# Performance work log

Hardware: AMD Instinct MI355X
Metric: run time of the kernel (lower is better)

## Reference

```python
import jax, jax.numpy as jnp
import numpy as np
from math import sqrt

B, L, DM, H, NL, INTER = 4, 2048, 256, 8, 3, 16
E = DM // H
FACTOR = 5


def _ln(x, g, b, eps=1e-5):
    m = x.mean(-1, keepdims=True)
    v = ((x - m) ** 2).mean(-1, keepdims=True)
    return (x - m) * jax.lax.rsqrt(v + eps) * g + b


def _prob_attn(q, k, v, rkey):
    # q,k,v: [B,H,L,E]; ProbAttention with mask_flag=False (as in AttentionLayer)
    Bq, Hq, Lq, Eq = q.shape
    Lk = k.shape[2]
    U = min(FACTOR * int(np.ceil(np.log(Lk))), Lk)   # sample_k
    u = min(FACTOR * int(np.ceil(np.log(Lq))), Lq)   # n_top
    # random K indices shared across B,H as in torch randint(L_K,(L_Q,sample_k))
    idx = jax.random.randint(rkey, (Lq, U), 0, Lk)
    k_samp = k[:, :, idx, :]                                   # [B,H,Lq,U,E]
    qk_samp = jnp.einsum('bhle,bhlue->bhlu', q, k_samp)        # [B,H,Lq,U]
    M = qk_samp.max(-1) - qk_samp.sum(-1) / Lk                 # sparsity score
    _, top = jax.lax.top_k(M, u)                               # [B,H,u]
    q_red = jnp.take_along_axis(q, top[..., None], axis=2)     # [B,H,u,E]
    scores = jnp.einsum('bhue,bhke->bhuk', q_red, k) * (1.0 / sqrt(Eq))
    attn = jax.nn.softmax(scores, axis=-1)
    upd = jnp.einsum('bhuk,bhkd->bhud', attn, v)               # [B,H,u,E]
    # initial context = mean of V broadcast over queries (non-masked branch)
    ctx = jnp.broadcast_to(v.mean(axis=2, keepdims=True), (Bq, Hq, Lq, Eq))
    bi = jnp.arange(Bq)[:, None, None]
    hi = jnp.arange(Hq)[None, :, None]
    ctx = ctx.at[bi, hi, top].set(upd)
    return ctx.transpose(0, 2, 1, 3)                           # [B,L,H,E]


def _enc_layer(x, wq, bq, wk, bk, wv, bv, wo, bo, c1w, c1b, c2w, c2b, g1, b1, g2, b2, rkey):
    Bx, Lx, _ = x.shape
    qh = (x @ wq.T + bq).reshape(Bx, Lx, H, E).transpose(0, 2, 1, 3)
    kh = (x @ wk.T + bk).reshape(Bx, Lx, H, E).transpose(0, 2, 1, 3)
    vh = (x @ wv.T + bv).reshape(Bx, Lx, H, E).transpose(0, 2, 1, 3)
    ctx = _prob_attn(qh, kh, vh, rkey).reshape(Bx, Lx, DM)
    x = _ln(x + ctx @ wo.T + bo, g1, b1)
    y = jax.nn.relu(jnp.einsum('bld,fd->blf', x, c1w) + c1b)   # 1x1 conv
    y = jnp.einsum('blf,df->bld', y, c2w) + c2b                # 1x1 conv
    return _ln(x + y, g2, b2)


def _distill(x, w, cb, g, b):
    # circular Conv1d(k=3,pad=1) + BatchNorm1d (train stats) + ELU; MaxPool(k=1) = identity
    xt = x.transpose(0, 2, 1)                                  # [B,C,L]
    xp = jnp.concatenate([xt[..., -1:], xt, xt[..., :1]], axis=-1)
    y = jax.lax.conv_general_dilated(xp, w, (1,), 'VALID',
                                     dimension_numbers=('NCH', 'OIH', 'NCH')) + cb[None, :, None]
    m = y.mean(axis=(0, 2), keepdims=True)
    v = y.var(axis=(0, 2), keepdims=True)                      # biased var, torch BN training
    y = jax.nn.elu((y - m) * jax.lax.rsqrt(v + 1e-5) * g[None, :, None] + b[None, :, None])
    return y.transpose(0, 2, 1)


def _forward(x, wq, bq, wk, bk, wv, bv, wo, bo, c1w, c1b, c2w, c2b,
             ln1g, ln1b, ln2g, ln2b, dcw, dcb, bng, bnb, fng, fnb):
    base = jax.random.key(42)
    for i in range(NL - 1):
        x = _enc_layer(x, wq[i], bq[i], wk[i], bk[i], wv[i], bv[i], wo[i], bo[i],
                       c1w[i], c1b[i], c2w[i], c2b[i], ln1g[i], ln1b[i], ln2g[i], ln2b[i],
                       jax.random.fold_in(base, i))
        x = _distill(x, dcw[i], dcb[i], bng[i], bnb[i])
    i = NL - 1
    x = _enc_layer(x, wq[i], bq[i], wk[i], bk[i], wv[i], bv[i], wo[i], bo[i],
                   c1w[i], c1b[i], c2w[i], c2b[i], ln1g[i], ln1b[i], ln2g[i], ln2b[i],
                   jax.random.fold_in(base, i))
    return _ln(x, fng, fnb)


def setup_inputs():
    key = jax.random.key(0)
    ks = jax.random.split(key, 10)
    g = lambda k, shp, s: jax.random.normal(k, shp, jnp.float32) * s
    z = lambda shp: jnp.zeros(shp, jnp.float32)
    o = lambda shp: jnp.ones(shp, jnp.float32)
    return {
        'x': g(ks[0], (B, L, DM), 1.0),
        'wq': g(ks[1], (NL, DM, DM), 0.03), 'bq': z((NL, DM)),
        'wk': g(ks[2], (NL, DM, DM), 0.03), 'bk': z((NL, DM)),
        'wv': g(ks[3], (NL, DM, DM), 0.03), 'bv': z((NL, DM)),
        'wo': g(ks[4], (NL, DM, DM), 0.03), 'bo': z((NL, DM)),
        'c1w': g(ks[5], (NL, INTER, DM), 0.05), 'c1b': z((NL, INTER)),
        'c2w': g(ks[6], (NL, DM, INTER), 0.05), 'c2b': z((NL, DM)),
        'ln1g': o((NL, DM)), 'ln1b': z((NL, DM)),
        'ln2g': o((NL, DM)), 'ln2b': z((NL, DM)),
        'dcw': g(ks[7], (NL - 1, DM, DM, 3), 0.02), 'dcb': z((NL - 1, DM)),
        'bng': o((NL - 1, DM)), 'bnb': z((NL - 1, DM)),
        'fng': o((DM,)), 'fnb': z((DM,)),
    }


def reference(x, wq, bq, wk, bk, wv, bv, wo, bo, c1w, c1b, c2w, c2b,
              ln1g, ln1b, ln2g, ln2b, dcw, dcb, bng, bnb, fng, fnb):
    return _forward(x, wq, bq, wk, bk, wv, bv, wo, bo, c1w, c1b, c2w, c2b,
                    ln1g, ln1b, ln2g, ln2b, dcw, dcb, bng, bnb, fng, fnb)
```

## Files before the change

### kernel.cpp

```cpp
#include <hip/hip_runtime.h>
#include <stdint.h>

#define BB 4
#define LL 2048
#define DMM 256
#define HH 8
#define EE 32
#define NLL 3
#define ITR 16
#define UU 40
#define KC 16
#define KCH 128
#define ROWS (BB*LL)
#define NELEM (ROWS*DMM)
#define OTR 32

typedef __attribute__((ext_vector_type(8))) short short8;
typedef __attribute__((ext_vector_type(4))) float f32x4;
typedef unsigned long long u64;

#define GLDS16(g, l)                                                        \
  __builtin_amdgcn_global_load_lds(                                         \
      (const __attribute__((address_space(1))) uint32_t*)(g),               \
      (__attribute__((address_space(3))) uint32_t*)(l), 16, 0, 0)

__device__ __forceinline__ float bfbits(unsigned short u) {
  return __uint_as_float(((uint32_t)u) << 16);
}
__device__ __forceinline__ unsigned short f2b(float f) {
  uint32_t u = __float_as_uint(f);
  uint32_t r = (u + 0x7FFFu + ((u >> 16) & 1u)) >> 16;
  return (unsigned short)r;
}

__host__ __device__ inline void threefry2x32(uint32_t k0, uint32_t k1,
                                             uint32_t x0, uint32_t x1,
                                             uint32_t* o0, uint32_t* o1) {
  uint32_t ks2 = k0 ^ k1 ^ 0x1BD11BDAu;
  x0 += k0; x1 += k1;
#define TFR(r) { x0 += x1; x1 = (x1 << (r)) | (x1 >> (32 - (r))); x1 ^= x0; }
  TFR(13) TFR(15) TFR(26) TFR(6)
  x0 += k1;  x1 += ks2 + 1u;
  TFR(17) TFR(29) TFR(16) TFR(24)
  x0 += ks2; x1 += k0 + 2u;
  TFR(13) TFR(15) TFR(26) TFR(6)
  x0 += k0;  x1 += k1 + 3u;
  TFR(17) TFR(29) TFR(16) TFR(24)
  x0 += k1;  x1 += ks2 + 4u;
  TFR(13) TFR(15) TFR(26) TFR(6)
  x0 += ks2; x1 += k0 + 5u;
#undef TFR
  *o0 = x0; *o1 = x1;
}

__device__ __forceinline__ float wave_sum(float v) {
#pragma unroll
  for (int off = 32; off > 0; off >>= 1) v += __shfl_xor(v, off);
  return v;
}

struct CvtArgs {
  const void* src[23];
  float* dstF[23];
  unsigned short* dstB[23];
  unsigned short* dstL[23];
  int n[23];
  int blkStart[24];
  unsigned short* dcwT;
  float* vmpZ;
  int* flagOut;
};
__global__ __launch_bounds__(256) void mega_cvt(CvtArgs a) {
  __shared__ int cnt;
  if (threadIdx.x == 0) cnt = 0;
  __syncthreads();
  {
    const unsigned short* u = (const unsigned short*)a.src[0];
    int bad = 0;
#pragma unroll
    for (int rep = 0; rep < 2; ++rep) {
      float v = bfbits(u[threadIdx.x + 256 * rep]);
      float av = fabsf(v);
      bool ok = (v == 0.0f) || (av > 1e-4f && av < 100.0f);
      if (!ok) bad++;
    }
    if (bad) atomicAdd(&cnt, bad);
  }
  __syncthreads();
  int isf32 = (cnt > 25) ? 1 : 0;

  int bid = blockIdx.x;
  if (bid == a.blkStart[23]) {
    for (int t = threadIdx.x; t < BB * DMM; t += 256) a.vmpZ[t] = 0.f;
    if (threadIdx.x == 0) *a.flagOut = isf32;
    return;
  }
  int i = 0;
  while (i < 22 && bid >= a.blkStart[i + 1]) ++i;
  int e = (bid - a.blkStart[i]) * 256 + (int)threadIdx.x;
  if (e >= a.n[i]) return;
  float v; unsigned short rw;
  if (isf32) { v = ((const float*)a.src[i])[e]; rw = f2b(v); }
  else       { rw = ((const unsigned short*)a.src[i])[e]; v = bfbits(rw); }
  a.dstF[i][e] = v;
  if (a.dstB[i]) a.dstB[i][e] = rw;
  if (a.dstL[i]) a.dstL[i][e] = f2b(v - bfbits(rw));
  if (i == 17) {
    int ly = e / 196608;
    int r = e - ly * 196608;
    int n = r / 768;
    int rem = r - n * 768;
    int k = rem / 3, t = rem - k * 3;
    a.dcwT[ly * 196608 + t * 65536 + n * 256 + k] = rw;
  }
}

struct QKVArgs {
  const unsigned short* W[3];
  const float* bias[3];
  float* Cq;
  float* Ck;
  unsigned short* Cv;
  float* vmp;
};
__global__ __launch_bounds__(256) void gemm_qkv(const unsigned short* __restrict__ Ahi,
                                                const unsigned short* __restrict__ Alo,
                                                QKVArgs qa) {
  __shared__ __attribute__((aligned(16))) unsigned short AsH[128][32];
  __shared__ __attribute__((aligned(16))) unsigned short AsL[128][32];
  __shared__ __attribute__((aligned(16))) unsigned short Bs[64][32];
  int z = blockIdx.z;
  const unsigned short* W = qa.W[z];
  const float* bias = qa.bias[z];
  bool twoPass = (z < 2);
  int bm = blockIdx.x * 128, bn = blockIdx.y * 64;
  int tid = threadIdx.x;
  int wv = tid >> 6, lane = tid & 63;
  int wm = wv >> 1, wn = wv & 1;
  int l15 = lane & 15, quad = lane >> 4;
  int lrow = lane >> 2, lseg = lane & 3;
  f32x4 acc[4][2];
#pragma unroll
  for (int i = 0; i < 4; ++i)
#pragma unroll
    for (int j = 0; j < 2; ++j) acc[i][j] = (f32x4){0.f, 0.f, 0.f, 0.f};
  for (int k0 = 0; k0 < 256; k0 += 32) {
    __syncthreads();
#pragma unroll
    for (int s = 0; s < 2; ++s) {
      int brow = (wv + s * 4) * 16;
      size_t goff = (size_t)(bm + brow + lrow) * 256 + k0 + lseg * 8;
      GLDS16(Ahi + goff, &AsH[brow][0]);
      if (twoPass) GLDS16(Alo + goff, &AsL[brow][0]);
    }
    {
      int brow = wv * 16;
      GLDS16(W + (size_t)(bn + brow + lrow) * 256 + k0 + lseg * 8, &Bs[brow][0]);
    }
    __syncthreads();
    short8 ah[4], bfr[2];
#pragma unroll
    for (int mt = 0; mt < 4; ++mt)
      ah[mt] = *(const short8*)(&AsH[wm * 64 + mt * 16 + l15][quad * 8]);
#pragma unroll
    for (int nt = 0; nt < 2; ++nt)
      bfr[nt] = *(const short8*)(&Bs[wn * 32 + nt * 16 + l15][quad * 8]);
#pragma unroll
    for (int mt = 0; mt < 4; ++mt)
#pragma unroll
      for (int nt = 0; nt < 2; ++nt)
        acc[mt][nt] = __builtin_amdgcn_mfma_f32_16x16x32_bf16(ah[mt], bfr[nt],
                                                              acc[mt][nt], 0, 0, 0);
    if (twoPass) {
      short8 al[4];
#pragma unroll
      for (int mt = 0; mt < 4; ++mt)
        al[mt] = *(const short8*)(&AsL[wm * 64 + mt * 16 + l15][quad * 8]);
#pragma unroll
      for (int mt = 0; mt < 4; ++mt)
#pragma unroll
        for (int nt = 0; nt < 2; ++nt)
          acc[mt][nt] = __builtin_amdgcn_mfma_f32_16x16x32_bf16(al[mt], bfr[nt],
                                                                acc[mt][nt], 0, 0, 0);
    }
  }
  float* C = (z == 0) ? qa.Cq : qa.Ck;
#pragma unroll
  for (int nt = 0; nt < 2; ++nt) {
    int n = bn + wn * 32 + nt * 16 + l15;
    float bv = bias[n];
    float csum = 0.f;
#pragma unroll
    for (int mt = 0; mt < 4; ++mt)
#pragma unroll
      for (int r = 0; r < 4; ++r) {
        int m = bm + wm * 64 + mt * 16 + quad * 4 + r;
        float val = acc[mt][nt][r] + bv;
        if (z < 2) {
          C[(size_t)m * 256 + n] = val;
        } else {
          qa.Cv[(size_t)m * 256 + n] = f2b(val);
          csum += val;
        }
      }
    if (z == 2) {
      csum += __shfl_xor(csum, 16);
      csum += __shfl_xor(csum, 32);
      if (quad == 0) {
        int b = bm >> 11;
        atomicAdd(&qa.vmp[b * DMM + n], csum);
      }
    }
  }
}

__global__ __launch_bounds__(512) void oproj_tail(const float* __restrict__ vmp,
                                                  const unsigned char* __restrict__ mapb,
                                                  const float* __restrict__ pm,
                                                  const float* __restrict__ pl,
                                                  const float* __restrict__ po,
                                                  const unsigned short* __restrict__ W,
                                                  const float* __restrict__ bias,
                                                  const float* __restrict__ X,
                                                  const float* __restrict__ g1,
                                                  const float* __restrict__ b1ln,
                                                  const float* __restrict__ w1,
                                                  const float* __restrict__ b1,
                                                  const float* __restrict__ w2,
                                                  const float* __restrict__ b2,
                                                  const float* __restrict__ g2,
                                                  const float* __restrict__ b2ln,
                                                  float* __restrict__ Out,
                                                  unsigned short* __restrict__ OutB,
                                                  unsigned short* __restrict__ OutL,
                                                  const float* __restrict__ fing,
                                                  const float* __restrict__ finb,
                                                  void* __restrict__ finOut,
                                                  const int* __restrict__ flag,
                                                  float* __restrict__ stpZ,
                                                  float* __restrict__ stp2Z) {
  __shared__ __attribute__((aligned(16))) unsigned short As[OTR][DMM];
  __shared__ __attribute__((aligned(16))) unsigned short Bs[256][32];
  __shared__ float Cs[OTR][DMM];
  __shared__ float xs[8][DMM];
  int tid = threadIdx.x;
  if (blockIdx.x == 0 && tid < DMM) {
    stpZ[tid] = 0.f;
    stp2Z[tid] = 0.f;
  }
  int bm = blockIdx.x * OTR;
  int wv = tid >> 6, lane = tid & 63;
  int l15 = lane & 15, quad = lane >> 4;
  int b = bm >> 11, l0 = bm & 2047;
  const float invL = 1.0f / (float)LL;

#pragma unroll
  for (int uu = 0; uu < 2; ++uu) {
    int u = tid * 2 + uu;
    int arow = u >> 5;
    int sub = u & 31;
    int h = sub >> 2, adg = sub & 3;
    int bh = b * HH + h;
    int l = l0 + arow;
    int q = (int)mapb[bh * 2048 + l];
    unsigned short outv[8];
    if (q) {
      size_t base = ((size_t)bh * UU + (q - 1)) * KC;
      float Mx = -1e30f;
#pragma unroll
      for (int kc = 0; kc < KC; ++kc) Mx = fmaxf(Mx, pm[base + kc]);
      float Ls = 0.f;
      float sc[KC];
#pragma unroll
      for (int kc = 0; kc < KC; ++kc) {
        sc[kc] = expf(pm[base + kc] - Mx);
        Ls += pl[base + kc] * sc[kc];
      }
      float inv = 1.0f / Ls;
#pragma unroll
      for (int j = 0; j < 8; ++j) {
        int dl = adg * 8 + j;
        float o = 0.f;
#pragma unroll
        for (int kc = 0; kc < KC; ++kc) o += po[(base + kc) * 32 + dl] * sc[kc];
        outv[j] = f2b(o * inv);
      }
    } else {
      const float* vp = vmp + b * DMM + h * EE + adg * 8;
#pragma unroll
      for (int j = 0; j < 8; ++j) outv[j] = f2b(vp[j] * invL);
    }
    *(uint4*)(&As[arow][h * EE + adg * 8]) = *(const uint4*)outv;
  }
  __syncthreads();

  f32x4 acc[2][2];
#pragma unroll
  for (int i = 0; i < 2; ++i)
#pragma unroll
    for (int j = 0; j < 2; ++j) acc[i][j] = (f32x4){0.f, 0.f, 0.f, 0.f};
  for (int k0 = 0; k0 < 256; k0 += 32) {
    if (k0) __syncthreads();
    {
      int lrw = lane >> 2, lsg = lane & 3;
#pragma unroll
      for (int s = 0; s < 2; ++s) {
        int brow = s * 128 + wv * 16;
        GLDS16(W + (size_t)(brow + lrw) * 256 + k0 + lsg * 8, &Bs[brow][0]);
      }
    }
    __syncthreads();
    short8 af[2], bfr[2];
#pragma unroll
    for (int mt = 0; mt < 2; ++mt)
      af[mt] = *(const short8*)(&As[mt * 16 + l15][k0 + quad * 8]);
#pragma unroll
    for (int nt = 0; nt < 2; ++nt)
      bfr[nt] = *(const short8*)(&Bs[wv * 32 + nt * 16 + l15][quad * 8]);
#pragma unroll
    for (int mt = 0; mt < 2; ++mt)
#pragma unroll
      for (int nt = 0; nt < 2; ++nt)
        acc[mt][nt] = __builtin_amdgcn_mfma_f32_16x16x32_bf16(af[mt], bfr[nt],
                                                              acc[mt][nt], 0, 0, 0);
  }
#pragma unroll
  for (int nt = 0; nt < 2; ++nt) {
    int n = wv * 32 + nt * 16 + l15;
    float bv = bias[n];
#pragma unroll
    for (int mt = 0; mt < 2; ++mt)
#pragma unroll
      for (int r = 0; r < 4; ++r)
        Cs[mt * 16 + quad * 4 + r][n] = acc[mt][nt][r] + bv;
  }
  __syncthreads();
  for (int rr = 0; rr < 4; ++rr) {
    int lr = wv * 4 + rr;
    size_t row = (size_t)bm + lr;
    const float* xr = X + row * DMM;
    const float* tr = Cs[lr];
    float v[4];
#pragma unroll
    for (int i = 0; i < 4; ++i) v[i] = xr[lane + 64 * i] + tr[lane + 64 * i];
    float s = wave_sum(v[0] + v[1] + v[2] + v[3]);
    float m = s * (1.0f / (float)DMM);
    float sq = 0.f;
#pragma unroll
    for (int i = 0; i < 4; ++i) { float d = v[i] - m; sq += d * d; }
    sq = wave_sum(sq);
    float rstd = rsqrtf(sq * (1.0f / (float)DMM) + 1e-5f);
    float xv[4];
#pragma unroll
    for (int i = 0; i < 4; ++i) {
      int d = lane + 64 * i;
      xv[i] = (v[i] - m) * rstd * g1[d] + b1ln[d];
      xs[wv][d] = xv[i];
    }
    __syncthreads();
    int f = lane & 15, qtr = lane >> 4;
    const float* w1p = w1 + f * DMM + qtr * 64;
    const float* xq = &xs[wv][qtr * 64];
    float pacc = 0.f;
#pragma unroll 8
    for (int d = 0; d < 64; ++d) pacc += xq[d] * w1p[d];
    pacc += __shfl_xor(pacc, 16);
    pacc += __shfl_xor(pacc, 32);
    float y1 = fmaxf(pacc + b1[f], 0.0f);
    float y1v[16];
#pragma unroll
    for (int ff = 0; ff < 16; ++ff) y1v[ff] = __shfl(y1, ff);
#pragma unroll
    for (int i = 0; i < 4; ++i) {
      int d = lane + 64 * i;
      const float* w2p = w2 + d * ITR;
      float a = b2[d];
#pragma unroll
      for (int ff = 0; ff < 16; ++ff) a += y1v[ff] * w2p[ff];
      v[i] = xv[i] + a;
    }
    s = wave_sum(v[0] + v[1] + v[2] + v[3]);
    m = s * (1.0f / (float)DMM);
    sq = 0.f;
#pragma unroll
    for (int i = 0; i < 4; ++i) { float d = v[i] - m; sq += d * d; }
    sq = wave_sum(sq);
    rstd = rsqrtf(sq * (1.0f / (float)DMM) + 1e-5f);
    float vv[4];
#pragma unroll
    for (int i = 0; i < 4; ++i) {
      int d = lane + 64 * i;
      float val = (v[i] - m) * rstd * g2[d] + b2ln[d];
      vv[i] = val;
      Out[row * DMM + d] = val;
      unsigned short hi = f2b(val);
      OutB[row * DMM + d] = hi;
      OutL[row * DMM + d] = f2b(val - bfbits(hi));
    }
    if (finOut) {
      s = wave_sum(vv[0] + vv[1] + vv[2] + vv[3]);
      m = s * (1.0f / (float)DMM);
      sq = 0.f;
#pragma unroll
      for (int i = 0; i < 4; ++i) { float d = vv[i] - m; sq += d * d; }
      sq = wave_sum(sq);
      rstd = rsqrtf(sq * (1.0f / (float)DMM) + 1e-5f);
      int isf32 = *flag;
#pragma unroll
      for (int i = 0; i < 4; ++i) {
        int d = lane + 64 * i;
        float val = (vv[i] - m) * rstd * fing[d] + finb[d];
        if (isf32) ((float*)finOut)[row * DMM + d] = val;
        else       ((unsigned short*)finOut)[row * DMM + d] = f2b(val);
      }
    }
  }
}

__global__ __launch_bounds__(256) void gemm_conv(const unsigned short* __restrict__ A,
                                                 const unsigned short* __restrict__ W,
                                                 const float* __restrict__ bias,
                                                 float* __restrict__ C,
                                                 float* __restrict__ stp,
                                                 float* __restrict__ stp2) {
  __shared__ __attribute__((aligned(16))) unsigned short As[80][32];
  __shared__ __attribute__((aligned(16))) unsigned short Bs[192][32];
  int bm = blockIdx.x * 64, bn = blockIdx.y * 64;
  int tid = threadIdx.x;
  int wv = tid >> 6, lane = tid & 63;
  int wm = wv >> 1, wn = wv & 1;
  int l15 = lane & 15, quad = lane >> 4;
  int lrow = lane >> 2, lseg = lane & 3;
  int bbase = bm & ~2047, l0 = bm & 2047;
  f32x4 acc[2][2];
#pragma unroll
  for (int i = 0; i < 2; ++i)
#pragma unroll
    for (int j = 0; j < 2; ++j) acc[i][j] = (f32x4){0.f, 0.f, 0.f, 0.f};
  for (int k0 = 0; k0 < 256; k0 += 32) {
    __syncthreads();
    for (int c = wv; c < 5; c += 4) {
      int i0 = c * 16;
      int l = (l0 - 1 + i0 + lrow + 2048) & 2047;
      GLDS16(A + (size_t)(bbase | l) * 256 + k0 + lseg * 8, &As[i0][0]);
    }
    for (int c = wv; c < 12; c += 4) {
      int i0 = c * 16;
      int tap = c >> 2, brow = (c & 3) * 16;
      GLDS16(W + (size_t)tap * 65536 + (size_t)(bn + brow + lrow) * 256 + k0 + lseg * 8,
             &Bs[i0][0]);
    }
    __syncthreads();
#pragma unroll
    for (int tap = 0; tap < 3; ++tap) {
      short8 af[2], bfr[2];
#pragma unroll
      for (int mt = 0; mt < 2; ++mt)
        af[mt] = *(const short8*)(&As[wm * 32 + mt * 16 + l15 + tap][quad * 8]);
#pragma unroll
      for (int nt = 0; nt < 2; ++nt)
        bfr[nt] = *(const short8*)(&Bs[tap * 64 + wn * 32 + nt * 16 + l15][quad * 8]);
#pragma unroll
      for (int mt = 0; mt < 2; ++mt)
#pragma unroll
        for (int nt = 0; nt < 2; ++nt)
          acc[mt][nt] = __builtin_amdgcn_mfma_f32_16x16x32_bf16(af[mt], bfr[nt],
                                                                acc[mt][nt], 0, 0, 0);
    }
  }
#pragma unroll
  for (int nt = 0; nt < 2; ++nt) {
    int n = bn + wn * 32 + nt * 16 + l15;
    float bv = bias[n];
    float s = 0.f, s2 = 0.f;
#pragma unroll
    for (int mt = 0; mt < 2; ++mt)
#pragma unroll
      for (int r = 0; r < 4; ++r) {
        int m = bm + wm * 32 + mt * 16 + quad * 4 + r;
        float val = acc[mt][nt][r] + bv;
        C[(size_t)m * 256 + n] = val;
        s += val;
        s2 += val * val;
      }
    s  += __shfl_xor(s, 16);   s  += __shfl_xor(s, 32);
    s2 += __shfl_xor(s2, 16);  s2 += __shfl_xor(s2, 32);
    if (quad == 0) {
      atomicAdd(&stp[n], s);
      atomicAdd(&stp2[n], s2);
    }
  }
}

__global__ __launch_bounds__(256) void m_kernel3(const float* __restrict__ Q,
                                                 const float* __restrict__ K,
                                                 uint32_t k20, uint32_t k21,
                                                 float* __restrict__ M) {
  int bid = blockIdx.x;
  int blk = (bid & 7) * 256 + (bid >> 3);
  int b = blk >> 9, lc = blk & 511;
  int wave = threadIdx.x >> 6, lane = threadIdx.x & 63;
  int l = lc * 4 + wave;
  int myidx = 0;
  if (lane < UU) {
    int j = l * UU + lane;
    uint32_t o0, o1;
    const int half = (LL * UU) / 2;
    if (j < half) {
      threefry2x32(k20, k21, (uint32_t)j, (uint32_t)(j + half), &o0, &o1);
      myidx = (int)(o0 & (LL - 1));
    } else {
      threefry2x32(k20, k21, (uint32_t)(j - half), (uint32_t)j, &o0, &o1);
      myidx = (int)(o1 & (LL - 1));
    }
  }
  float4 q4 = *(const float4*)(Q + ((size_t)(b * LL + l)) * DMM + lane * 4);
  const float* Kb = K + (size_t)b * LL * DMM;
  float mx = -1e30f, sm = 0.f;
#pragma unroll 8
  for (int u = 0; u < UU; ++u) {
    int kidx = __shfl(myidx, u);
    float4 k4 = *(const float4*)(Kb + (size_t)kidx * DMM + lane * 4);
    float s = q4.x * k4.x + q4.y * k4.y + q4.z * k4.z + q4.w * k4.w;
    s += __shfl_xor(s, 1);
    s += __shfl_xor(s, 2);
    s += __shfl_xor(s, 4);
    mx = fmaxf(mx, s);
    sm += s;
  }
  if ((lane & 7) == 0) {
    int h = lane >> 3;
    M[((size_t)(b * HH + h)) * LL + l] = mx - sm * (1.0f / (float)LL);
  }
}

__global__ __launch_bounds__(256) void attn_part(const float* __restrict__ Q,
                                                 const float* __restrict__ K,
                                                 const unsigned short* __restrict__ Vbf,
                                                 const float* __restrict__ M,
                                                 unsigned char* __restrict__ mapb,
                                                 float* __restrict__ pm,
                                                 float* __restrict__ pl,
                                                 float* __restrict__ po) {
  __shared__ float Qs[40][32];
  __shared__ unsigned short ps[40][KCH];
  __shared__ unsigned short Vs[KCH][40];
  __shared__ int qrows[40];
  __shared__ unsigned int hist[256];
  __shared__ unsigned int sA[256];
  __shared__ unsigned int sB[256];
  __shared__ unsigned int tbv;
  int kc = blockIdx.x, bh = blockIdx.y;
  int h = bh & 7, b = bh >> 3;
  int tid = threadIdx.x;
  int wv = tid >> 6, lane = tid & 63;

  {
    int row = tid >> 1, half = tid & 1;
    const unsigned short* vsrc =
        Vbf + (size_t)(b * LL + kc * KCH + row) * DMM + h * EE + half * 16;
    *(uint4*)(&Vs[row][half * 16]) = *(const uint4*)vsrc;
    *(uint4*)(&Vs[row][half * 16 + 8]) = *(const uint4*)(vsrc + 8);
  }
  int kk = tid & (KCH - 1), qh = tid >> 7;
  float4 kr[8];
  {
    const float4* kp =
        (const float4*)(K + ((size_t)(b * LL + kc * KCH + kk)) * DMM + h * EE);
#pragma unroll
    for (int j = 0; j < 8; ++j) kr[j] = kp[j];
  }

  u64 kreg[8];
#pragma unroll
  for (int r = 0; r < 8; ++r) {
    int l = tid + 256 * r;
    float v = M[(size_t)bh * LL + l];
    uint32_t bits = __float_as_uint(v);
    uint32_t kv = (bits & 0x80000000u) ? ~bits : (bits | 0x80000000u);
    kreg[r] = ((u64)kv << 32) | (uint32_t)(2047 - l);
  }
  u64 prefix = 0;
  int rank = UU;
  for (int round = 0; round < 8; ++round) {
    int shift = 56 - 8 * round;
    u64 maskTop = (round == 0) ? 0ull : (~0ull << (64 - 8 * round));
    hist[tid] = 0;
    __syncthreads();
#pragma unroll
    for (int r = 0; r < 8; ++r) {
      u64 k = kreg[r];
      if ((k & maskTop) == prefix)
        atomicAdd(&hist[(unsigned int)((k >> shift) & 0xFFu)], 1u);
    }
    __syncthreads();
    sA[tid] = hist[tid];
    __syncthreads();
    unsigned int* src = sA;
    unsigned int* dst = sB;
    for (int off = 1; off < 256; off <<= 1) {
      unsigned int v = src[tid] + ((tid + off < 256) ? src[tid + off] : 0u);
      dst[tid] = v;
      __syncthreads();
      unsigned int* tmpp = src; src = dst; dst = tmpp;
    }
    unsigned int Sb = src[tid];
    unsigned int Snext = (tid < 255) ? src[tid + 1] : 0u;
    if (Sb >= (unsigned int)rank && Snext < (unsigned int)rank) tbv = (unsigned int)tid;
    __syncthreads();
    unsigned int tb = tbv;
    unsigned int above = (tb < 255u) ? src[tb + 1] : 0u;
    rank -= (int)above;
    prefix |= ((u64)tb) << shift;
    __syncthreads();
  }
  u64 T = prefix;
  int myCnt = 0;
#pragma unroll
  for (int r = 0; r < 8; ++r) myCnt += (kreg[r] >= T) ? 1 : 0;
  sA[tid] = (unsigned int)myCnt;
  __syncthreads();
  {
    unsigned int* src = sA;
    unsigned int* dst = sB;
    for (int off = 1; off < 256; off <<= 1) {
      unsigned int v = src[tid] + ((tid >= off) ? src[tid - off] : 0u);
      dst[tid] = v;
      __syncthreads();
      unsigned int* tmpp = src; src = dst; dst = tmpp;
    }
    int pos = (int)src[tid] - myCnt;
    bool wmap = (kc == 0);
#pragma unroll
    for (int r = 0; r < 8; ++r) {
      u64 k = kreg[r];
      int l = 2047 - (int)(uint32_t)(k & 0xFFFFFFFFu);
      unsigned char mv = 0;
      if (k >= T) {
        qrows[pos] = l;
        mv = (unsigned char)(pos + 1);
        pos++;
      }
      if (wmap) mapb[bh * 2048 + l] = mv;
    }
  }
  __syncthreads();

  for (int t = tid; t < 40 * 32; t += 256) {
    int q = t >> 5, d = t & 31;
    Qs[q][d] = Q[((size_t)(b * LL + qrows[q])) * DMM + h * EE + d];
  }
  __syncthreads();
  {
    const float scale = 0.17677669529663687f;
    for (int q = qh * 20; q < qh * 20 + 20; ++q) {
      const float4* qp = (const float4*)Qs[q];
      float s = 0.f;
#pragma unroll
      for (int j = 0; j < 8; ++j) {
        float4 qv = qp[j];
        s += qv.x * kr[j].x + qv.y * kr[j].y + qv.z * kr[j].z + qv.w * kr[j].w;
      }
      ps[q][kk] = f2b(s * scale);
    }
  }
  __syncthreads();
  int kg = lane >> 5, d = lane & 31;
  for (int qq = 0; qq < 10; ++qq) {
    int q = wv * 10 + qq;
    float mx = fmaxf(bfbits(ps[q][lane]), bfbits(ps[q][lane + 64]));
#pragma unroll
    for (int off = 32; off > 0; off >>= 1) mx = fmaxf(mx, __shfl_xor(mx, off));
    float e0 = expf(bfbits(ps[q][lane]) - mx);
    float e1 = expf(bfbits(ps[q][lane + 64]) - mx);
    ps[q][lane] = f2b(e0);
    ps[q][lane + 64] = f2b(e1);
    float sum = wave_sum(e0 + e1);
    float o = 0.f;
#pragma unroll 8
    for (int j = 0; j < KCH / 2; ++j) {
      int r = 2 * j + kg;
      o += bfbits(ps[q][r]) * bfbits(Vs[r][d]);
    }
    o += __shfl_xor(o, 32);
    size_t base = ((size_t)bh * UU + q) * KC + kc;
    if (lane == 0) { pm[base] = mx; pl[base] = sum; }
    if (lane < 32) po[base * 32 + d] = o;
  }
}

__global__ __launch_bounds__(256) void bn_elu(const float* __restrict__ Y,
                                              const float* __restrict__ stp,
                                              const float* __restrict__ stp2,
                                              const float* __restrict__ g,
                                              const float* __restrict__ bb,
                                              float* __restrict__ X,
                                              unsigned short* __restrict__ XB,
                                              unsigned short* __restrict__ XL,
                                              float* __restrict__ vmpZ) {
  int gid = blockIdx.x * 256 + threadIdx.x;
  if (gid < BB * DMM) vmpZ[gid] = 0.f;
  int d = gid & 255;
  float mean = stp[d] * (1.0f / (float)ROWS);
  float var = stp2[d] * (1.0f / (float)ROWS) - mean * mean;
  float rstd = rsqrtf(var + 1e-5f);
  float v = (Y[gid] - mean) * rstd * g[d] + bb[d];
  float r = v > 0.f ? v : expm1f(v);
  X[gid] = r;
  unsigned short hi = f2b(r);
  XB[gid] = hi;
  XL[gid] = f2b(r - bfbits(hi));
}

extern "C" void kernel_launch(void* const* d_in, const int* in_sizes, int n_in,
                              void* d_out, int out_size, void* d_ws, size_t ws_size,
                              hipStream_t stream) {
  (void)in_sizes; (void)n_in; (void)out_size; (void)ws_size;

  float* xbuf = (float*)d_ws;
  float* kb   = xbuf + NELEM;
  float* qb   = kb + NELEM;
  float* tmp  = qb;
  float* Mbuf = qb + NELEM;
  float* vmp  = Mbuf + BB * HH * LL;
  float* stp  = vmp + BB * DMM;
  float* stp2 = stp + DMM;
  float* wp   = stp2 + DMM;
  const int wsz[23] = {
      NELEM,
      NLL * DMM * DMM, NLL * DMM,
      NLL * DMM * DMM, NLL * DMM,
      NLL * DMM * DMM, NLL * DMM,
      NLL * DMM * DMM, NLL * DMM,
      NLL * ITR * DMM, NLL * ITR,
      NLL * DMM * ITR, NLL * DMM,
      NLL * DMM, NLL * DMM,
      NLL * DMM, NLL * DMM,
      (NLL - 1) * DMM * DMM * 3, (NLL - 1) * DMM,
      (NLL - 1) * DMM, (NLL - 1) * DMM,
      DMM, DMM
  };
  float* fptr[23];
  fptr[0] = xbuf;
  for (int i = 1; i < 23; ++i) { fptr[i] = wp; wp += wsz[i]; }
  float* pm = wp;
  float* pl = pm + 32 * UU * KC;
  float* po = pl + 32 * UU * KC;
  unsigned short* xbf   = (unsigned short*)(po + 32 * UU * KC * 32);
  unsigned short* xlo   = xbf + NELEM;
  unsigned short* vbf   = xlo + NELEM;
  unsigned short* wqbf  = vbf + NELEM;
  unsigned short* wkbf  = wqbf + NLL * DMM * DMM;
  unsigned short* wvbf  = wkbf + NLL * DMM * DMM;
  unsigned short* wobf  = wvbf + NLL * DMM * DMM;
  unsigned short* dcwT  = wobf + NLL * DMM * DMM;
  u64* cand = (u64*)(dcwT + (NLL - 1) * 3 * DMM * DMM);
  int* topb = (int*)(cand + 256 * 40);
  int* flag = topb + BB * HH * UU;
  unsigned char* mapb = (unsigned char*)(flag + 1);

  CvtArgs ca;
  int totalBlk = 0;
  for (int i = 0; i < 23; ++i) {
    ca.src[i] = d_in[i];
    ca.dstF[i] = fptr[i];
    ca.dstB[i] = nullptr;
    ca.dstL[i] = nullptr;
    ca.n[i] = wsz[i];
    ca.blkStart[i] = totalBlk;
    totalBlk += (wsz[i] + 255) / 256;
  }
  ca.blkStart[23] = totalBlk;
  ca.dstB[0] = xbf;  ca.dstL[0] = xlo;
  ca.dstB[1] = wqbf;
  ca.dstB[3] = wkbf;
  ca.dstB[5] = wvbf;
  ca.dstB[7] = wobf;
  ca.dcwT = dcwT;
  ca.vmpZ = vmp;
  ca.flagOut = flag;
  mega_cvt<<<totalBlk + 1, 256, 0, stream>>>(ca);

  dim3 gqkv(ROWS / 128, DMM / 64, 3);
  dim3 g64(ROWS / 64, DMM / 64);

  for (int i = 0; i < NLL; ++i) {
    QKVArgs qa;
    qa.W[0] = wqbf + (size_t)i * DMM * DMM;
    qa.W[1] = wkbf + (size_t)i * DMM * DMM;
    qa.W[2] = wvbf + (size_t)i * DMM * DMM;
    qa.bias[0] = fptr[2] + i * DMM;
    qa.bias[1] = fptr[4] + i * DMM;
    qa.bias[2] = fptr[6] + i * DMM;
    qa.Cq = qb; qa.Ck = kb; qa.Cv = vbf;
    qa.vmp = vmp;
    gemm_qkv<<<gqkv, 256, 0, stream>>>(xbf, xlo, qa);

    uint32_t ki0, ki1, a0, a1, b0, b1;
    threefry2x32(0u, 42u, 0u, (uint32_t)i, &ki0, &ki1);
    threefry2x32(ki0, ki1, 0u, 2u, &a0, &a1);
    threefry2x32(ki0, ki1, 1u, 3u, &b0, &b1);
    (void)a0; (void)b0;

    m_kernel3<<<BB * 512, 256, 0, stream>>>(qb, kb, a1, b1, Mbuf);
    attn_part<<<dim3(KC, BB * HH), 256, 0, stream>>>(qb, kb, vbf, Mbuf, mapb,
                                                     pm, pl, po);

    bool last = (i == NLL - 1);
    oproj_tail<<<ROWS / OTR, 512, 0, stream>>>(
        vmp, mapb, pm, pl, po,
        wobf + (size_t)i * DMM * DMM, fptr[8] + i * DMM,
        xbuf,
        fptr[13] + i * DMM, fptr[14] + i * DMM,
        fptr[9] + (size_t)i * ITR * DMM, fptr[10] + i * ITR,
        fptr[11] + (size_t)i * DMM * ITR, fptr[12] + i * DMM,
        fptr[15] + i * DMM, fptr[16] + i * DMM,
        xbuf, xbf, xlo,
        fptr[21], fptr[22], last ? d_out : nullptr, flag, stp, stp2);

    if (!last) {
      gemm_conv<<<g64, 256, 0, stream>>>(xbf, dcwT + (size_t)i * 3 * DMM * DMM,
                                         fptr[18] + i * DMM, tmp, stp, stp2);
      bn_elu<<<NELEM / 256, 256, 0, stream>>>(tmp, stp, stp2, fptr[19] + i * DMM,
                                              fptr[20] + i * DMM, xbuf, xbf, xlo, vmp);
    }
  }
}
```

Measured before the change: 487.2 us.

## Shrink top-k radix select to 43-bit keys and use wavefront shuffle scans

The per-block top-u selection in attn_part now packs the sparsity score and the row index into a 43-bit key, so the radix select runs 6 rounds instead of 8. The 256-wide shared-memory Hillis-Steele scans, which needed a barrier per step, are replaced with 64-lane shuffle scans plus a small per-wave total combine. One trailing barrier per round is also dropped. The aim is to cut the many block-wide barriers and shared-memory round trips in the selection phase. In exchange it relies on careful reasoning about reuse of shared buffers across rounds and about the reduced index field width.

```diff
diff --git a/kernel.cpp b/kernel.cpp
--- a/kernel.cpp
+++ b/kernel.cpp
@@ -548,7 +548,7 @@
   __shared__ int qrows[40];
   __shared__ unsigned int hist[256];
   __shared__ unsigned int sA[256];
-  __shared__ unsigned int sB[256];
+  __shared__ unsigned int wtot[4];
   __shared__ unsigned int tbv;
   int kc = blockIdx.x, bh = blockIdx.y;
   int h = bh & 7, b = bh >> 3;
@@ -578,13 +578,13 @@
     float v = M[(size_t)bh * LL + l];
     uint32_t bits = __float_as_uint(v);
     uint32_t kv = (bits & 0x80000000u) ? ~bits : (bits | 0x80000000u);
-    kreg[r] = ((u64)kv << 32) | (uint32_t)(2047 - l);
+    kreg[r] = ((u64)kv << 11) | (uint32_t)(2047 - l);
   }
   u64 prefix = 0;
   int rank = UU;
-  for (int round = 0; round < 8; ++round) {
-    int shift = 56 - 8 * round;
-    u64 maskTop = (round == 0) ? 0ull : (~0ull << (64 - 8 * round));
+  for (int round = 0; round < 6; ++round) {
+    int shift = 40 - 8 * round;
+    u64 maskTop = (round == 0) ? 0ull : (~0ull << (48 - 8 * round));
     hist[tid] = 0;
     __syncthreads();
 #pragma unroll
@@ -594,47 +594,52 @@
         atomicAdd(&hist[(unsigned int)((k >> shift) & 0xFFu)], 1u);
     }
     __syncthreads();
-    sA[tid] = hist[tid];
-    __syncthreads();
-    unsigned int* src = sA;
-    unsigned int* dst = sB;
-    for (int off = 1; off < 256; off <<= 1) {
-      unsigned int v = src[tid] + ((tid + off < 256) ? src[tid + off] : 0u);
-      dst[tid] = v;
-      __syncthreads();
-      unsigned int* tmpp = src; src = dst; dst = tmpp;
-    }
-    unsigned int Sb = src[tid];
-    unsigned int Snext = (tid < 255) ? src[tid + 1] : 0u;
+    unsigned int s = hist[tid];
+#pragma unroll
+    for (int off = 1; off < 64; off <<= 1) {
+      unsigned int t = __shfl_down(s, off);
+      if (lane + off < 64) s += t;
+    }
+    if (lane == 0) wtot[wv] = s;
+    __syncthreads();
+    unsigned int add = 0;
+#pragma unroll
+    for (int w = 0; w < 4; ++w)
+      if (w > wv) add += wtot[w];
+    sA[tid] = s + add;
+    __syncthreads();
+    unsigned int Sb = sA[tid];
+    unsigned int Snext = (tid < 255) ? sA[tid + 1] : 0u;
     if (Sb >= (unsigned int)rank && Snext < (unsigned int)rank) tbv = (unsigned int)tid;
     __syncthreads();
     unsigned int tb = tbv;
-    unsigned int above = (tb < 255u) ? src[tb + 1] : 0u;
+    unsigned int above = (tb < 255u) ? sA[tb + 1] : 0u;
     rank -= (int)above;
     prefix |= ((u64)tb) << shift;
-    __syncthreads();
   }
   u64 T = prefix;
   int myCnt = 0;
 #pragma unroll
   for (int r = 0; r < 8; ++r) myCnt += (kreg[r] >= T) ? 1 : 0;
-  sA[tid] = (unsigned int)myCnt;
-  __syncthreads();
   {
-    unsigned int* src = sA;
-    unsigned int* dst = sB;
-    for (int off = 1; off < 256; off <<= 1) {
-      unsigned int v = src[tid] + ((tid >= off) ? src[tid - off] : 0u);
-      dst[tid] = v;
-      __syncthreads();
-      unsigned int* tmpp = src; src = dst; dst = tmpp;
-    }
-    int pos = (int)src[tid] - myCnt;
+    unsigned int p = (unsigned int)myCnt;
+#pragma unroll
+    for (int off = 1; off < 64; off <<= 1) {
+      unsigned int t = __shfl_up(p, off);
+      if (lane >= off) p += t;
+    }
+    if (lane == 63) wtot[wv] = p;
+    __syncthreads();
+    unsigned int addp = 0;
+#pragma unroll
+    for (int w = 0; w < 4; ++w)
+      if (w < wv) addp += wtot[w];
+    int pos = (int)(p + addp) - myCnt;
     bool wmap = (kc == 0);
 #pragma unroll
     for (int r = 0; r < 8; ++r) {
       u64 k = kreg[r];
-      int l = 2047 - (int)(uint32_t)(k & 0xFFFFFFFFu);
+      int l = 2047 - (int)(uint32_t)(k & 0x7FFu);
       unsigned char mv = 0;
       if (k >= T) {
         qrows[pos] = l;
```

Measured after the change: 477.7 us. No clear change (-2.0%).
